# Performance work log

Hardware: AMD Instinct MI355X
Metric: run time of the kernel (lower is better)

## Reference

```python
import jax, jax.numpy as jnp
import numpy as np

NUM_HEADS = 8
ROPE_THETA = 10.0


def _axial_angles(height, width, head_dim, theta):
    # frequencies: 1/theta^(arange(0, head_dim, 4)[:head_dim//4] / head_dim)  -> [head_dim//4]
    hd4 = head_dim // 4
    freqs = 1.0 / (theta ** (np.arange(0, head_dim, 4)[:hd4].astype(np.float32) / head_dim))
    t = np.arange(height * width)
    t_x = (t % width).astype(np.float32)
    t_y = (t // width).astype(np.float32)
    ang_x = np.outer(t_x, freqs)  # [n, head_dim//4]
    ang_y = np.outer(t_y, freqs)
    return jnp.asarray(ang_x), jnp.asarray(ang_y)


def _apply_rope(x, cos, sin):
    # x: [b, h, n, half]; cos/sin: [n, half//2]; complex-pair rotation on last dim
    xr = x[..., 0::2]
    xi = x[..., 1::2]
    out_r = xr * cos - xi * sin
    out_i = xr * sin + xi * cos
    return jnp.stack([out_r, out_i], axis=-1).reshape(x.shape)


def setup_inputs() -> dict:
    key = jax.random.key(0)
    ks = jax.random.split(key, 5)
    b, n, c = 4, 16384, 512
    x = jax.random.normal(ks[0], (b, n, c), dtype=jnp.float32)
    w_qkv = jax.random.normal(ks[1], (c, 3 * c), dtype=jnp.float32) * 0.02
    b_qkv = jax.random.normal(ks[2], (3 * c,), dtype=jnp.float32) * 0.02
    w_proj = jax.random.normal(ks[3], (c, c), dtype=jnp.float32) * 0.02
    b_proj = jax.random.normal(ks[4], (c,), dtype=jnp.float32) * 0.02
    return {"x": x, "w_qkv": w_qkv, "b_qkv": b_qkv, "w_proj": w_proj, "b_proj": b_proj,
            "height": 128, "width": 128}


def reference(x, w_qkv, b_qkv, w_proj, b_proj, height, width):
    b, n, c = x.shape
    h = NUM_HEADS
    hd = c // h
    half = hd // 2

    qkv = (x @ w_qkv + b_qkv).reshape(b, n, 3, h, hd).transpose(2, 0, 3, 1, 4)
    q, k, v = qkv[0], qkv[1], qkv[2]  # each [b, h, n, hd]

    ang_x, ang_y = _axial_angles(height, width, hd, ROPE_THETA)
    cx, sx = jnp.cos(ang_x), jnp.sin(ang_x)
    cy, sy = jnp.cos(ang_y), jnp.sin(ang_y)

    q = jnp.concatenate([_apply_rope(q[..., :half], cx, sx),
                         _apply_rope(q[..., half:], cy, sy)], axis=-1)
    k = jnp.concatenate([_apply_rope(k[..., :half], cx, sx),
                         _apply_rope(k[..., half:], cy, sy)], axis=-1)

    # kernel feature map: elu(x) + 1 (positive)
    q = jax.nn.elu(q) + 1.0
    k = jax.nn.elu(k) + 1.0

    # linear attention: O(n d^2)
    kv = jnp.einsum('bhnd,bhne->bhde', k, v)
    out = jnp.einsum('bhnd,bhde->bhne', q, kv)
    z = 1.0 / (jnp.einsum('bhnd,bhd->bhn', q, k.sum(axis=2)) + 1e-6)
    out = out * z[..., None]

    out = out.transpose(0, 2, 1, 3).reshape(b, n, c)
    return out @ w_proj + b_proj
```

## Files before the change

### kernel.cpp

```cpp
#include <hip/hip_runtime.h>
#include <math.h>

#define BATCH 4
#define NTOK  16384
#define CDIM  512
#define NH    8
#define HD    64
#define M_ROWS (BATCH*NTOK)
#define KDIM  512

typedef _Float16 f16;
typedef _Float16 f16x8 __attribute__((ext_vector_type(8)));
typedef _Float16 f16x4 __attribute__((ext_vector_type(4)));
typedef _Float16 f16x2 __attribute__((ext_vector_type(2)));
typedef float    f32x4 __attribute__((ext_vector_type(4)));

__device__ __forceinline__ void load_lds16(const void* g, void* l) {
    __builtin_amdgcn_global_load_lds(
        (const __attribute__((address_space(1))) void*)g,
        (__attribute__((address_space(3))) void*)l, 16, 0, 0);
}

__global__ __launch_bounds__(256)
void prep(const float* __restrict__ x, f16* __restrict__ xh,
          const float* __restrict__ wq, f16* __restrict__ wqt,
          const float* __restrict__ wp, f16* __restrict__ wpt,
          float* __restrict__ tab)
{
    const int bid = blockIdx.x;
    const int tid = threadIdx.x;
    __shared__ float lds[32][33];

    if (bid < 16384) {
        int i = bid * 256 + tid;
        float4 a = *(const float4*)&x[(size_t)i * 8];
        float4 b = *(const float4*)&x[(size_t)i * 8 + 4];
        f16x8 o;
        o[0]=(f16)a.x; o[1]=(f16)a.y; o[2]=(f16)a.z; o[3]=(f16)a.w;
        o[4]=(f16)b.x; o[5]=(f16)b.y; o[6]=(f16)b.z; o[7]=(f16)b.w;
        *(f16x8*)&xh[(size_t)i * 8] = o;
    } else if (bid < 16384 + 1024) {
        int tb = bid - 16384;
        const float* src; f16* dst; int N;
        if (tb < 768) { src = wq; dst = wqt; N = 1536; }
        else          { tb -= 768; src = wp; dst = wpt; N = 512; }
        int kt  = tb & 15;
        int ntl = tb >> 4;
        int tx = tid & 31, ty = tid >> 5;
        #pragma unroll
        for (int i = 0; i < 4; i++)
            lds[ty + 8 * i][tx] = src[(size_t)(kt * 32 + ty + 8 * i) * N + ntl * 32 + tx];
        __syncthreads();
        #pragma unroll
        for (int i = 0; i < 4; i++) {
            int p  = ty + 8 * i;
            int tc = (p < 16) ? (2 * p) : (2 * (p - 16) + 1);
            dst[(size_t)(ntl * 32 + p) * 512 + kt * 32 + tx] = (f16)lds[tx][tc];
        }
    } else {
        int idx = (bid - (16384 + 1024)) * 256 + tid;
        int t   = (idx >> 4) & 127;
        int fi  = idx & 15;
        float freq = powf(10.f, -(float)fi / 16.f);
        float s, c;
        sincosf((float)t * freq, &s, &c);
        tab[idx * 2]     = c;
        tab[idx * 2 + 1] = s;
    }
}

template<int MODE>
__global__ __launch_bounds__(256, 2)
void gemm_f16(const f16* __restrict__ A, const f16* __restrict__ Bt,
              const float* __restrict__ bias,
              float* __restrict__ Co,
              f16* __restrict__ qd, f16* __restrict__ kd, f16* __restrict__ vd,
              const float* __restrict__ tab, int ncol_tiles)
{
    __shared__ f16 As[128 * 64];
    __shared__ f16 Bs[128 * 64];
    const int tid  = threadIdx.x;
    const int lane = tid & 63;
    const int wave = tid >> 6;
    const int wy = wave >> 1, wx = wave & 1;

    const int bid = blockIdx.x;
    const int xcd = bid & 7;
    const int idx = bid >> 3;
    const int ct  = idx % ncol_tiles;
    const int rt  = (idx / ncol_tiles) * 8 + xcd;
    const int row0 = rt * 128;
    const int col0 = ct * 128;

    const int l15 = lane & 15;
    const int l4  = lane >> 4;

    f32x4 acc[4][4];
    #pragma unroll
    for (int mt = 0; mt < 4; mt++)
        #pragma unroll
        for (int nt = 0; nt < 4; nt++)
            acc[mt][nt] = (f32x4){0.f, 0.f, 0.f, 0.f};

    const int pbase = wave * 256;

    for (int k0 = 0; k0 < KDIM; k0 += 64) {
        #pragma unroll
        for (int i = 0; i < 4; i++) {
            int p  = pbase + i * 64 + lane;
            int m  = p >> 3;
            int jp = p & 7;
            int j  = jp ^ (m & 7);
            load_lds16(&A [(size_t)(row0 + m) * KDIM + k0 + j * 8],
                       &As[(pbase + i * 64) * 8]);
            load_lds16(&Bt[(size_t)(col0 + m) * KDIM + k0 + j * 8],
                       &Bs[(pbase + i * 64) * 8]);
        }
        __syncthreads();

        #pragma unroll
        for (int s = 0; s < 2; s++) {
            f16x8 af[4], bf[4];
            #pragma unroll
            for (int t = 0; t < 4; t++) {
                int ra = wy * 64 + t * 16 + l15;
                int rb = wx * 64 + t * 16 + l15;
                int ca = ((s << 2) | l4) ^ (ra & 7);
                int cb = ((s << 2) | l4) ^ (rb & 7);
                af[t] = *(const f16x8*)&As[ra * 64 + ca * 8];
                bf[t] = *(const f16x8*)&Bs[rb * 64 + cb * 8];
            }
            #pragma unroll
            for (int mt = 0; mt < 4; mt++)
                #pragma unroll
                for (int nt = 0; nt < 4; nt++)
                    acc[mt][nt] = __builtin_amdgcn_mfma_f32_16x16x32_f16(af[mt], bf[nt], acc[mt][nt], 0, 0, 0);
        }
        __syncthreads();
    }

    if (MODE == 0) {
        #pragma unroll
        for (int q = 0; q < 2; q++) {
            int B32 = (col0 + wx * 64 + q * 32) >> 5;
            int t0c = B32 * 32 + 2 * l15;
            float bv0 = bias[t0c];
            float bv1 = bias[t0c + 1];
            #pragma unroll
            for (int mt = 0; mt < 4; mt++)
                #pragma unroll
                for (int r = 0; r < 4; r++) {
                    int row = row0 + wy * 64 + mt * 16 + l4 * 4 + r;
                    float2 o2;
                    o2.x = acc[mt][2 * q][r]     + bv0;
                    o2.y = acc[mt][2 * q + 1][r] + bv1;
                    *(float2*)&Co[(size_t)row * CDIM + t0c] = o2;
                }
        }
    } else {
        const int which = col0 >> 9;
        f16* dst = (which == 0) ? qd : (which == 1) ? kd : vd;
        const float2* tab2 = (const float2*)tab;
        #pragma unroll
        for (int q = 0; q < 2; q++) {
            int B32  = (col0 + wx * 64 + q * 32) >> 5;
            int t0   = B32 * 32 + 2 * l15;
            int c512 = t0 & 511;
            float bv0 = bias[t0];
            float bv1 = bias[t0 + 1];
            int isy  = B32 & 1;
            const float2* ct = tab2 + isy * 2048 + l15;
            if (which == 2) {
                #pragma unroll
                for (int mt = 0; mt < 4; mt++)
                    #pragma unroll
                    for (int r = 0; r < 4; r++) {
                        int row = row0 + wy * 64 + mt * 16 + l4 * 4 + r;
                        f16x2 pk;
                        pk[0] = (f16)(acc[mt][2 * q][r]     + bv0);
                        pk[1] = (f16)(acc[mt][2 * q + 1][r] + bv1);
                        *(f16x2*)&dst[(size_t)row * CDIM + c512] = pk;
                    }
            } else {
                #pragma unroll
                for (int mt = 0; mt < 4; mt++)
                    #pragma unroll
                    for (int r = 0; r < 4; r++) {
                        int row = row0 + wy * 64 + mt * 16 + l4 * 4 + r;
                        int tok = row & (NTOK - 1);
                        int t   = isy ? (tok >> 7) : (tok & 127);
                        float2 cs = ct[t * 16];
                        float xr = acc[mt][2 * q][r]     + bv0;
                        float xi = acc[mt][2 * q + 1][r] + bv1;
                        float o_r = xr * cs.x - xi * cs.y;
                        float o_i = xr * cs.y + xi * cs.x;
                        o_r = (o_r > 0.f) ? o_r + 1.f : __expf(o_r);
                        o_i = (o_i > 0.f) ? o_i + 1.f : __expf(o_i);
                        f16x2 pk; pk[0] = (f16)o_r; pk[1] = (f16)o_i;
                        *(f16x2*)&dst[(size_t)row * CDIM + c512] = pk;
                    }
            }
        }
    }
}

__global__ __launch_bounds__(256, 4)
void kv_kernel(const f16* __restrict__ kk, const f16* __restrict__ vv,
               float* __restrict__ kvt, float* __restrict__ ksum)
{
    int bh = blockIdx.x;
    int b = bh >> 3, h = bh & 7;
    int t0 = blockIdx.y * 1024;
    __shared__ float ks[64][68];
    __shared__ float vs[64][68];
    int tid = threadIdx.x;
    const int wave = tid >> 6;
    const int lane = tid & 63;
    const int ly = lane >> 3;
    const int lx = lane & 7;
    const int o  = (tid & 7) * 8;

    float acc[8][8];
    float ksacc[8];
    #pragma unroll
    for (int r = 0; r < 8; r++) { ksacc[r] = 0.f;
        #pragma unroll
        for (int j = 0; j < 8; j++) acc[r][j] = 0.f; }

    const size_t rowbase = (size_t)b * NTOK;
    for (int tt = t0; tt < t0 + 1024; tt += 64) {
        #pragma unroll
        for (int i = 0; i < 2; i++) {
            int idx = tid + i * 256;
            int tok = idx >> 3;
            size_t g = (rowbase + tt + tok) * CDIM + h * HD + o;
            f16x8 k8 = *(const f16x8*)&kk[g];
            f16x8 v8 = *(const f16x8*)&vv[g];
            float4 klo = {(float)k8[0], (float)k8[1], (float)k8[2], (float)k8[3]};
            float4 khi = {(float)k8[4], (float)k8[5], (float)k8[6], (float)k8[7]};
            float4 vlo = {(float)v8[0], (float)v8[1], (float)v8[2], (float)v8[3]};
            float4 vhi = {(float)v8[4], (float)v8[5], (float)v8[6], (float)v8[7]};
            *(float4*)&ks[tok][o]     = klo;
            *(float4*)&ks[tok][o + 4] = khi;
            *(float4*)&vs[tok][o]     = vlo;
            *(float4*)&vs[tok][o + 4] = vhi;
            ksacc[0] += klo.x; ksacc[1] += klo.y; ksacc[2] += klo.z; ksacc[3] += klo.w;
            ksacc[4] += khi.x; ksacc[5] += khi.y; ksacc[6] += khi.z; ksacc[7] += khi.w;
        }
        __syncthreads();
        #pragma unroll
        for (int t5 = 0; t5 < 16; t5++) {
            int t = wave * 16 + t5;
            float4 ka0 = *(const float4*)&ks[t][ly * 8];
            float4 ka1 = *(const float4*)&ks[t][ly * 8 + 4];
            float4 va0 = *(const float4*)&vs[t][lx * 8];
            float4 va1 = *(const float4*)&vs[t][lx * 8 + 4];
            float ka[8] = {ka0.x, ka0.y, ka0.z, ka0.w, ka1.x, ka1.y, ka1.z, ka1.w};
            float va[8] = {va0.x, va0.y, va0.z, va0.w, va1.x, va1.y, va1.z, va1.w};
            #pragma unroll
            for (int r = 0; r < 8; r++)
                #pragma unroll
                for (int j = 0; j < 8; j++) acc[r][j] += ka[r] * va[j];
        }
        __syncthreads();
    }

    float* ksl = &vs[0][0];
    {
        float4 a = {ksacc[0], ksacc[1], ksacc[2], ksacc[3]};
        float4 c = {ksacc[4], ksacc[5], ksacc[6], ksacc[7]};
        *(float4*)&ksl[tid * 8]     = a;
        *(float4*)&ksl[tid * 8 + 4] = c;
    }
    float* red = &ks[0][0];
    #pragma unroll
    for (int w = 0; w < 4; w++) {
        if (wave == w) {
            #pragma unroll
            for (int j = 0; j < 8; j++) {
                int base = (lx * 8 + j) * 64 + ly * 8;
                float4 lo = {acc[0][j], acc[1][j], acc[2][j], acc[3][j]};
                float4 hi = {acc[4][j], acc[5][j], acc[6][j], acc[7][j]};
                if (w == 0) {
                    *(float4*)&red[base]     = lo;
                    *(float4*)&red[base + 4] = hi;
                } else {
                    float4 p0 = *(const float4*)&red[base];
                    float4 p1 = *(const float4*)&red[base + 4];
                    p0.x += lo.x; p0.y += lo.y; p0.z += lo.z; p0.w += lo.w;
                    p1.x += hi.x; p1.y += hi.y; p1.z += hi.z; p1.w += hi.w;
                    *(float4*)&red[base]     = p0;
                    *(float4*)&red[base + 4] = p1;
                }
            }
        }
        __syncthreads();
    }
    #pragma unroll
    for (int i = 0; i < 16; i++) {
        int idx = tid + i * 256;
        atomicAdd(&kvt[bh * 4096 + idx], red[idx]);
    }
    if (tid < 64) {
        float s = 0.f;
        #pragma unroll
        for (int m = 0; m < 32; m++)
            s += ksl[((tid >> 3) + m * 8) * 8 + (tid & 7)];
        atomicAdd(&ksum[bh * 64 + tid], s);
    }
}

__global__ void kv_pack(const float* __restrict__ kvt,
                        f16* __restrict__ kvhi, f16* __restrict__ kvlo)
{
    int idx = blockIdx.x * 256 + threadIdx.x;
    float4 v = *(const float4*)&kvt[idx * 4];
    f16x4 hi, lo;
    hi[0] = (f16)v.x; lo[0] = (f16)(v.x - (float)hi[0]);
    hi[1] = (f16)v.y; lo[1] = (f16)(v.y - (float)hi[1]);
    hi[2] = (f16)v.z; lo[2] = (f16)(v.z - (float)hi[2]);
    hi[3] = (f16)v.w; lo[3] = (f16)(v.w - (float)hi[3]);
    *(f16x4*)&kvhi[idx * 4] = hi;
    *(f16x4*)&kvlo[idx * 4] = lo;
}

__global__ __launch_bounds__(256, 4)
void attn_kernel(const f16* __restrict__ q, const f16* __restrict__ kvhi,
                 const f16* __restrict__ kvlo, const float* __restrict__ ksum,
                 f16* __restrict__ attnh)
{
    int bh = blockIdx.x;
    int b = bh >> 3, h = bh & 7;
    int rc = blockIdx.y;
    int tid = threadIdx.x;
    const int lane = tid & 63;
    const int wave = tid >> 6;
    const int l15 = lane & 15;
    const int l4  = lane >> 4;

    f16x8 bhi[2][4], blo[2][4];
    #pragma unroll
    for (int s = 0; s < 2; s++)
        #pragma unroll
        for (int nt = 0; nt < 4; nt++) {
            int e = nt * 16 + l15;
            size_t gb = (size_t)bh * 4096 + e * 64 + s * 32 + l4 * 8;
            bhi[s][nt] = *(const f16x8*)&kvhi[gb];
            blo[s][nt] = *(const f16x8*)&kvlo[gb];
        }
    float ksA[2][8];
    #pragma unroll
    for (int s = 0; s < 2; s++)
        #pragma unroll
        for (int j = 0; j < 8; j++)
            ksA[s][j] = ksum[bh * 64 + s * 32 + l4 * 8 + j];

    const size_t qbase = ((size_t)b * NTOK + rc * 256 + wave * 64) * CDIM + (size_t)h * HD;

    #pragma unroll
    for (int mt = 0; mt < 4; mt++) {
        f16x8 af[2];
        #pragma unroll
        for (int s = 0; s < 2; s++)
            af[s] = *(const f16x8*)&q[qbase + (size_t)(mt * 16 + l15) * CDIM + s * 32 + l4 * 8];

        float zp = 0.f;
        #pragma unroll
        for (int s = 0; s < 2; s++)
            #pragma unroll
            for (int j = 0; j < 8; j++)
                zp += (float)af[s][j] * ksA[s][j];
        zp += __shfl_xor(zp, 16, 64);
        zp += __shfl_xor(zp, 32, 64);
        float zinv = 1.f / (zp + 1e-6f);

        f32x4 acc[4];
        #pragma unroll
        for (int nt = 0; nt < 4; nt++) acc[nt] = (f32x4){0.f, 0.f, 0.f, 0.f};
        #pragma unroll
        for (int s = 0; s < 2; s++)
            #pragma unroll
            for (int nt = 0; nt < 4; nt++) {
                acc[nt] = __builtin_amdgcn_mfma_f32_16x16x32_f16(af[s], bhi[s][nt], acc[nt], 0, 0, 0);
                acc[nt] = __builtin_amdgcn_mfma_f32_16x16x32_f16(af[s], blo[s][nt], acc[nt], 0, 0, 0);
            }

        #pragma unroll
        for (int r = 0; r < 4; r++) {
            float zr = __shfl(zinv, l4 * 4 + r, 64);
            size_t orow = qbase + (size_t)(mt * 16 + l4 * 4 + r) * CDIM;
            #pragma unroll
            for (int nt = 0; nt < 4; nt++)
                attnh[orow + nt * 16 + l15] = (f16)(acc[nt][r] * zr);
        }
    }
}

extern "C" void kernel_launch(void* const* d_in, const int* in_sizes, int n_in,
                              void* d_out, int out_size, void* d_ws, size_t ws_size,
                              hipStream_t stream)
{
    const float* x      = (const float*)d_in[0];
    const float* w_qkv  = (const float*)d_in[1];
    const float* b_qkv  = (const float*)d_in[2];
    const float* w_proj = (const float*)d_in[3];
    const float* b_proj = (const float*)d_in[4];
    float* out = (float*)d_out;
    char*  ws  = (char*)d_ws;

    const size_t NCB = (size_t)M_ROWS * CDIM * sizeof(f16);
    f16*   xh   = (f16*)(ws);
    f16*   qh   = (f16*)(ws + NCB * 1);
    f16*   kh   = (f16*)(ws + NCB * 2);
    f16*   vh   = (f16*)(ws + NCB * 3);
    f16*   wqt  = (f16*)(ws + NCB * 4);
    f16*   wpt  = (f16*)(ws + NCB * 4 + (1536 * 512) * sizeof(f16));
    float* tab  = (float*)(ws + NCB * 4 + (1536 * 512 + 512 * 512) * sizeof(f16));
    float* kvp  = tab + 8192;
    float* ksum = kvp + 32 * 4096;
    f16*   kvhi = (f16*)(ksum + 32 * 64);
    f16*   kvlo = kvhi + 32 * 4096;

    hipMemsetAsync(kvp, 0, (32 * 4096 + 32 * 64) * sizeof(float), stream);
    prep<<<16384 + 1024 + 16, 256, 0, stream>>>(x, xh, w_qkv, wqt, w_proj, wpt, tab);

    gemm_f16<1><<<6144, 256, 0, stream>>>(xh, wqt, b_qkv,
                                          nullptr, qh, kh, vh, tab, 12);
    kv_kernel<<<dim3(32, 16), 256, 0, stream>>>(kh, vh, kvp, ksum);
    kv_pack<<<128, 256, 0, stream>>>(kvp, kvhi, kvlo);
    attn_kernel<<<dim3(32, 64), 256, 0, stream>>>(qh, kvhi, kvlo, ksum, vh);
    gemm_f16<0><<<2048, 256, 0, stream>>>(vh, wpt, b_proj,
                                          out, nullptr, nullptr, nullptr, nullptr, 4);
}
```

Before: 537.6 us.

## Double-buffer LDS tiles in GEMM with async prefetch two stages ahead

The GEMM main loop now keeps two LDS buffers for A and B. Global-to-LDS loads for the tile two steps ahead are issued right after the current tile's fragments are read into registers, so they overlap the MFMA work. Manual vmcnt/lgkmcnt waits and raw barriers replace __syncthreads, and s_setprio raises wave priority around the MFMA block. LDS use doubles to 64KB per block, which may reduce occupancy at the requested 2 blocks per CU, and the hand-written wait counts must match the number of outstanding loads.

```diff
diff --git a/kernel.cpp b/kernel.cpp
--- a/kernel.cpp
+++ b/kernel.cpp
@@ -77,8 +77,8 @@
               f16* __restrict__ qd, f16* __restrict__ kd, f16* __restrict__ vd,
               const float* __restrict__ tab, int ncol_tiles)
 {
-    __shared__ f16 As[128 * 64];
-    __shared__ f16 Bs[128 * 64];
+    __shared__ f16 As[2][128 * 64];
+    __shared__ f16 Bs[2][128 * 64];
     const int tid  = threadIdx.x;
     const int lane = tid & 63;
     const int wave = tid >> 6;
@@ -104,7 +104,7 @@
 
     const int pbase = wave * 256;
 
-    for (int k0 = 0; k0 < KDIM; k0 += 64) {
+    auto stage = [&](int buf, int k0) {
         #pragma unroll
         for (int i = 0; i < 4; i++) {
             int p  = pbase + i * 64 + lane;
@@ -112,31 +112,55 @@
             int jp = p & 7;
             int j  = jp ^ (m & 7);
             load_lds16(&A [(size_t)(row0 + m) * KDIM + k0 + j * 8],
-                       &As[(pbase + i * 64) * 8]);
+                       &As[buf][(pbase + i * 64) * 8]);
             load_lds16(&Bt[(size_t)(col0 + m) * KDIM + k0 + j * 8],
-                       &Bs[(pbase + i * 64) * 8]);
-        }
-        __syncthreads();
-
-        #pragma unroll
-        for (int s = 0; s < 2; s++) {
-            f16x8 af[4], bf[4];
-            #pragma unroll
-            for (int t = 0; t < 4; t++) {
-                int ra = wy * 64 + t * 16 + l15;
-                int rb = wx * 64 + t * 16 + l15;
+                       &Bs[buf][(pbase + i * 64) * 8]);
+        }
+    };
+
+    constexpr int NT = KDIM / 64;
+
+    stage(0, 0);
+    stage(1, 64);
+    asm volatile("s_waitcnt vmcnt(8)" ::: "memory");
+    __builtin_amdgcn_s_barrier();
+
+    #pragma unroll
+    for (int t = 0; t < NT; ++t) {
+        const int cur = t & 1;
+        f16x8 af[2][4], bf[2][4];
+        #pragma unroll
+        for (int s = 0; s < 2; s++)
+            #pragma unroll
+            for (int u = 0; u < 4; u++) {
+                int ra = wy * 64 + u * 16 + l15;
+                int rb = wx * 64 + u * 16 + l15;
                 int ca = ((s << 2) | l4) ^ (ra & 7);
                 int cb = ((s << 2) | l4) ^ (rb & 7);
-                af[t] = *(const f16x8*)&As[ra * 64 + ca * 8];
-                bf[t] = *(const f16x8*)&Bs[rb * 64 + cb * 8];
+                af[s][u] = *(const f16x8*)&As[cur][ra * 64 + ca * 8];
+                bf[s][u] = *(const f16x8*)&Bs[cur][rb * 64 + cb * 8];
             }
+        asm volatile("s_waitcnt lgkmcnt(0)" ::: "memory");
+        if (t + 2 < NT) {
+            __builtin_amdgcn_s_barrier();
+            stage(cur, (t + 2) * 64);
+        }
+        __builtin_amdgcn_s_setprio(1);
+        #pragma unroll
+        for (int s = 0; s < 2; s++)
             #pragma unroll
             for (int mt = 0; mt < 4; mt++)
                 #pragma unroll
                 for (int nt = 0; nt < 4; nt++)
-                    acc[mt][nt] = __builtin_amdgcn_mfma_f32_16x16x32_f16(af[mt], bf[nt], acc[mt][nt], 0, 0, 0);
-        }
-        __syncthreads();
+                    acc[mt][nt] = __builtin_amdgcn_mfma_f32_16x16x32_f16(af[s][mt], bf[s][nt], acc[mt][nt], 0, 0, 0);
+        __builtin_amdgcn_s_setprio(0);
+        if (t + 1 < NT) {
+            if (t + 2 < NT)
+                asm volatile("s_waitcnt vmcnt(8)" ::: "memory");
+            else
+                asm volatile("s_waitcnt vmcnt(0)" ::: "memory");
+            __builtin_amdgcn_s_barrier();
+        }
     }
 
     if (MODE == 0) {
```

Measured after the change: 546.3 us. No clear change (+1.6%).
